# Performance work log

Measured on AMD Instinct MI355X. Metric: run time of the kernel, lower is better.

## Reference

```python
import jax, jax.numpy as jnp
import numpy as np

N_HEAD = 10

def setup_inputs() -> dict:
    key = jax.random.key(0)
    k1, k2, k3 = jax.random.split(key, 3)
    n_embd = 640
    x = jax.random.normal(k1, (4, 2048, n_embd), dtype=jnp.float32)
    w_qkv = jax.random.normal(k2, (3 * n_embd, n_embd), dtype=jnp.float32) * (1.0 / np.sqrt(n_embd))
    w_proj = jax.random.normal(k3, (n_embd, n_embd), dtype=jnp.float32) * (1.0 / np.sqrt(n_embd))
    return {"x": x, "w_qkv": w_qkv, "w_proj": w_proj}

def reference(x, w_qkv, w_proj):
    bsz, seqlen, n_embd = x.shape
    head_dim = n_embd // N_HEAD
    qkv = jnp.einsum('bsd,ed->bse', x, w_qkv)  # [B,S,3E]
    q, k, v = jnp.split(qkv, 3, axis=2)
    # [B,H,S,Dh]
    q = q.reshape(bsz, seqlen, N_HEAD, head_dim).transpose(0, 2, 1, 3)
    k = k.reshape(bsz, seqlen, N_HEAD, head_dim).transpose(0, 2, 1, 3)
    v = v.reshape(bsz, seqlen, N_HEAD, head_dim).transpose(0, 2, 1, 3)
    scale = 1.0 / np.sqrt(head_dim).astype(np.float32)
    scores = jnp.einsum('bhqd,bhkd->bhqk', q, k) * scale
    causal = jnp.tril(jnp.ones((seqlen, seqlen), dtype=bool))
    scores = jnp.where(causal, scores, jnp.finfo(scores.dtype).min)
    attn = jax.nn.softmax(scores, axis=-1)
    y = jnp.einsum('bhqk,bhkd->bhqd', attn, v)
    y = y.transpose(0, 2, 1, 3).reshape(bsz, seqlen, n_embd)
    return jnp.einsum('bsd,ed->bse', y, w_proj)
```

## Files before the change

### kernel.cpp

```cpp
#include <hip/hip_runtime.h>

#define BB 4
#define SS 2048
#define EE 640
#define NHH 10
#define DHH 64
#define MTOK 8192
#define E33 1920

#define LDST 72

typedef float f32x4 __attribute__((ext_vector_type(4)));
typedef __bf16 bf16x8 __attribute__((ext_vector_type(8)));
typedef unsigned short u16;
typedef u16 u16x4 __attribute__((ext_vector_type(4)));

__device__ inline u16 f2bf(float f) {
  unsigned u = __builtin_bit_cast(unsigned, f);
  u += 0x7fffu + ((u >> 16) & 1u);
  return (u16)(u >> 16);
}

__global__ void convert_kernel(const float* __restrict__ in, u16* __restrict__ out, int n4) {
  int i = blockIdx.x * blockDim.x + threadIdx.x;
  if (i < n4) {
    float4 v = ((const float4*)in)[i];
    u16x4 o = { f2bf(v.x), f2bf(v.y), f2bf(v.z), f2bf(v.w) };
    ((u16x4*)out)[i] = o;
  }
}

__global__ __launch_bounds__(256) void gemm_qkv(
    const u16* __restrict__ A, const u16* __restrict__ Bt,
    u16* __restrict__ qb, u16* __restrict__ kb, u16* __restrict__ vt) {
  __shared__ __align__(16) u16 As[128 * LDST];
  __shared__ __align__(16) u16 Bs[128 * LDST];
  const int t = threadIdx.x;
  const int m0 = blockIdx.y * 128;
  const int n0 = blockIdx.x * 128;
  const int w = t >> 6, lane = t & 63, n16 = lane & 15, quad = lane >> 4;
  const int wm = w >> 1, wn = w & 1;

  f32x4 acc[4][4];
  for (int i = 0; i < 4; i++)
    for (int j = 0; j < 4; j++) acc[i][j] = f32x4{0.f, 0.f, 0.f, 0.f};

  for (int kt = 0; kt < 10; ++kt) {
    __syncthreads();
    for (int i = 0; i < 4; ++i) {
      int c = i * 256 + t;
      int row = c >> 3, col0 = (c & 7) * 8;
      *(bf16x8*)&As[row * LDST + col0] = *(const bf16x8*)&A[(m0 + row) * 640 + kt * 64 + col0];
      *(bf16x8*)&Bs[row * LDST + col0] = *(const bf16x8*)&Bt[(n0 + row) * 640 + kt * 64 + col0];
    }
    __syncthreads();
    for (int ks = 0; ks < 2; ++ks) {
      bf16x8 a[4], b[4];
      for (int mi = 0; mi < 4; mi++)
        a[mi] = *(const bf16x8*)&As[(wm * 64 + mi * 16 + n16) * LDST + ks * 32 + quad * 8];
      for (int ni = 0; ni < 4; ni++)
        b[ni] = *(const bf16x8*)&Bs[(wn * 64 + ni * 16 + n16) * LDST + ks * 32 + quad * 8];
      for (int mi = 0; mi < 4; mi++)
        for (int ni = 0; ni < 4; ni++)
          acc[mi][ni] = __builtin_amdgcn_mfma_f32_16x16x32_bf16(a[mi], b[ni], acc[mi][ni], 0, 0, 0);
    }
  }

  const int which = n0 / 640;
  for (int ni = 0; ni < 4; ni++) {
    int col = n0 + wn * 64 + ni * 16 + n16;
    int eh = col - which * 640;
    int h = eh >> 6, d = eh & 63;
    for (int mi = 0; mi < 4; mi++) {
      int tb = m0 + wm * 64 + mi * 16 + quad * 4;
      f32x4 c = acc[mi][ni];
      if (which == 2) {
        int b_ = tb >> 11, s_ = tb & 2047;
        u16x4 pk = { f2bf(c[0]), f2bf(c[1]), f2bf(c[2]), f2bf(c[3]) };
        *(u16x4*)&vt[((b_ * NHH + h) * DHH + d) * SS + s_] = pk;
      } else {
        u16* dst = (which == 0) ? qb : kb;
        for (int r = 0; r < 4; r++) {
          int tok = tb + r;
          int b_ = tok >> 11, s_ = tok & 2047;
          dst[((b_ * NHH + h) * SS + s_) * DHH + d] = f2bf(c[r]);
        }
      }
    }
  }
}

__global__ __launch_bounds__(256) void attn_kernel(
    const u16* __restrict__ qb, const u16* __restrict__ kb, const u16* __restrict__ vt,
    u16* __restrict__ y) {
  __shared__ __align__(16) u16 Ks[2][64 * LDST];
  __shared__ __align__(16) u16 Vs[2][64 * LDST];
  const int t = threadIdx.x;
  const int w = t >> 6, lane = t & 63, n16 = lane & 15, quad = lane >> 4;
  const int bh = blockIdx.x;
  const int qt = 31 - blockIdx.y;
  const int qb0 = qt * 64;
  const int b_ = bh / NHH, h = bh % NHH;

  bf16x8 aq[2];
  {
    const u16* qp = &qb[(bh * SS + qb0 + w * 16 + n16) * DHH];
    aq[0] = *(const bf16x8*)&qp[quad * 8];
    aq[1] = *(const bf16x8*)&qp[32 + quad * 8];
  }
  const int q_rel = w * 16 + n16;

  const int c1 = 256 + t;
  const int row0 = t >> 3,  col0 = (t & 7) * 8;
  const int row1 = c1 >> 3, col1 = (c1 & 7) * 8;
  auto perm = [](int k) {
    int p = k >> 5, rem = k & 31, qd = rem >> 3, tt = rem & 7;
    return ((p << 1) | (tt >> 2)) * 16 + qd * 4 + (tt & 3);
  };
  const int prow0 = perm(row0), prow1 = perm(row1);

  float4 fk0, fk1, fv0, fv1;
  fk0 = *(const float4*)&kb[(bh * SS + row0) * DHH + col0];
  fk1 = *(const float4*)&kb[(bh * SS + row1) * DHH + col1];
  fv0 = *(const float4*)&vt[(bh * DHH + row0) * SS + col0];
  fv1 = *(const float4*)&vt[(bh * DHH + row1) * SS + col1];
  *(float4*)&Ks[0][prow0 * LDST + col0] = fk0;
  *(float4*)&Ks[0][prow1 * LDST + col1] = fk1;
  *(float4*)&Vs[0][row0 * LDST + col0] = fv0;
  *(float4*)&Vs[0][row1 * LDST + col1] = fv1;

  float m_i = -1e30f, l_i = 0.f;
  f32x4 o[4];
  for (int db = 0; db < 4; db++) o[db] = f32x4{0.f, 0.f, 0.f, 0.f};

  for (int kt = 0; kt <= qt; ++kt) {
    __syncthreads();
    const int cur = kt & 1, nxt = cur ^ 1;
    if (kt < qt) {
      int kk = (kt + 1) * 64;
      fk0 = *(const float4*)&kb[(bh * SS + kk + row0) * DHH + col0];
      fk1 = *(const float4*)&kb[(bh * SS + kk + row1) * DHH + col1];
      fv0 = *(const float4*)&vt[(bh * DHH + row0) * SS + kk + col0];
      fv1 = *(const float4*)&vt[(bh * DHH + row1) * SS + kk + col1];
    }

    f32x4 sc[4];
    for (int nb = 0; nb < 4; nb++) {
      f32x4 c = f32x4{0.f, 0.f, 0.f, 0.f};
      for (int ks = 0; ks < 2; ks++) {
        bf16x8 ak = *(const bf16x8*)&Ks[cur][(nb * 16 + n16) * LDST + ks * 32 + quad * 8];
        c = __builtin_amdgcn_mfma_f32_16x16x32_bf16(ak, aq[ks], c, 0, 0, 0);
      }
      sc[nb] = c;
    }
    const bool diag = (kt == qt);
    for (int nb = 0; nb < 4; nb++)
      for (int r = 0; r < 4; r++) {
        float v = sc[nb][r] * 0.125f;
        int key = ((nb >> 1) << 5) + quad * 8 + ((nb & 1) << 2) + r;
        sc[nb][r] = (diag && key > q_rel) ? -1e30f : v;
      }

    float rm = -1e30f;
    for (int nb = 0; nb < 4; nb++)
      for (int r = 0; r < 4; r++) rm = fmaxf(rm, sc[nb][r]);
    rm = fmaxf(rm, __shfl_xor(rm, 16));
    rm = fmaxf(rm, __shfl_xor(rm, 32));
    float mnew = fmaxf(m_i, rm);
    float alpha = __expf(m_i - mnew);
    float p[4][4];
    float rs = 0.f;
    for (int nb = 0; nb < 4; nb++)
      for (int r = 0; r < 4; r++) { float pv = __expf(sc[nb][r] - mnew); p[nb][r] = pv; rs += pv; }
    rs += __shfl_xor(rs, 16);
    rs += __shfl_xor(rs, 32);
    l_i = l_i * alpha + rs;
    m_i = mnew;
    for (int db = 0; db < 4; db++)
      for (int r = 0; r < 4; r++) o[db][r] *= alpha;

    for (int p2 = 0; p2 < 2; p2++) {
      union { bf16x8 v; u16 s[8]; } bp;
      for (int j = 0; j < 4; j++) {
        bp.s[j]     = f2bf(p[2 * p2][j]);
        bp.s[4 + j] = f2bf(p[2 * p2 + 1][j]);
      }
      for (int db = 0; db < 4; db++) {
        bf16x8 av = *(const bf16x8*)&Vs[cur][(db * 16 + n16) * LDST + p2 * 32 + quad * 8];
        o[db] = __builtin_amdgcn_mfma_f32_16x16x32_bf16(av, bp.v, o[db], 0, 0, 0);
      }
    }

    if (kt < qt) {
      *(float4*)&Ks[nxt][prow0 * LDST + col0] = fk0;
      *(float4*)&Ks[nxt][prow1 * LDST + col1] = fk1;
      *(float4*)&Vs[nxt][row0 * LDST + col0] = fv0;
      *(float4*)&Vs[nxt][row1 * LDST + col1] = fv1;
    }
  }

  const float inv = 1.0f / l_i;
  const int tok = b_ * SS + qb0 + w * 16 + n16;
  for (int db = 0; db < 4; db++) {
    u16x4 pk = { f2bf(o[db][0] * inv), f2bf(o[db][1] * inv),
                 f2bf(o[db][2] * inv), f2bf(o[db][3] * inv) };
    *(u16x4*)&y[tok * EE + h * DHH + db * 16 + quad * 4] = pk;
  }
}

__global__ __launch_bounds__(256) void gemm_proj(
    const u16* __restrict__ A, const u16* __restrict__ Bt, float* __restrict__ out) {
  __shared__ __align__(16) u16 As[128 * LDST];
  __shared__ __align__(16) u16 Bs[128 * LDST];
  const int t = threadIdx.x;
  const int m0 = blockIdx.y * 128;
  const int n0 = blockIdx.x * 128;
  const int w = t >> 6, lane = t & 63, n16 = lane & 15, quad = lane >> 4;
  const int wm = w >> 1, wn = w & 1;

  f32x4 acc[4][4];
  for (int i = 0; i < 4; i++)
    for (int j = 0; j < 4; j++) acc[i][j] = f32x4{0.f, 0.f, 0.f, 0.f};

  for (int kt = 0; kt < 10; ++kt) {
    __syncthreads();
    for (int i = 0; i < 4; ++i) {
      int c = i * 256 + t;
      int row = c >> 3, col0 = (c & 7) * 8;
      *(bf16x8*)&As[row * LDST + col0] = *(const bf16x8*)&A[(m0 + row) * 640 + kt * 64 + col0];
      *(bf16x8*)&Bs[row * LDST + col0] = *(const bf16x8*)&Bt[(n0 + row) * 640 + kt * 64 + col0];
    }
    __syncthreads();
    for (int ks = 0; ks < 2; ++ks) {
      bf16x8 a[4], b[4];
      for (int mi = 0; mi < 4; mi++)
        a[mi] = *(const bf16x8*)&As[(wm * 64 + mi * 16 + n16) * LDST + ks * 32 + quad * 8];
      for (int ni = 0; ni < 4; ni++)
        b[ni] = *(const bf16x8*)&Bs[(wn * 64 + ni * 16 + n16) * LDST + ks * 32 + quad * 8];
      for (int mi = 0; mi < 4; mi++)
        for (int ni = 0; ni < 4; ni++)
          acc[mi][ni] = __builtin_amdgcn_mfma_f32_16x16x32_bf16(a[mi], b[ni], acc[mi][ni], 0, 0, 0);
    }
  }

  for (int ni = 0; ni < 4; ni++) {
    int col = n0 + wn * 64 + ni * 16 + n16;
    for (int mi = 0; mi < 4; mi++) {
      int rowb = m0 + wm * 64 + mi * 16 + quad * 4;
      f32x4 c = acc[mi][ni];
      for (int r = 0; r < 4; r++) out[(rowb + r) * 640 + col] = c[r];
    }
  }
}

extern "C" void kernel_launch(void* const* d_in, const int* in_sizes, int n_in,
                              void* d_out, int out_size, void* d_ws, size_t ws_size,
                              hipStream_t stream) {
  const float* x     = (const float*)d_in[0];
  const float* wqkv  = (const float*)d_in[1];
  const float* wproj = (const float*)d_in[2];
  float* out = (float*)d_out;

  char* ws = (char*)d_ws;
  u16* xb     = (u16*)(ws + 0);
  u16* wqkvb  = (u16*)(ws + 10485760);
  u16* wprojb = (u16*)(ws + 12943360);
  u16* qbuf   = (u16*)(ws + 13762560);
  u16* kbuf   = (u16*)(ws + 24248320);
  u16* vtb    = (u16*)(ws + 34734080);
  u16* ybuf   = (u16*)(ws + 45219840);

  convert_kernel<<<5120, 256, 0, stream>>>(x, xb, 5242880 / 4);
  convert_kernel<<<1200, 256, 0, stream>>>(wqkv, wqkvb, 1228800 / 4);
  convert_kernel<<<400, 256, 0, stream>>>(wproj, wprojb, 409600 / 4);

  gemm_qkv<<<dim3(15, 64), 256, 0, stream>>>(xb, wqkvb, qbuf, kbuf, vtb);
  attn_kernel<<<dim3(40, 32), 256, 0, stream>>>(qbuf, kbuf, vtb, ybuf);
  gemm_proj<<<dim3(5, 64), 256, 0, stream>>>(ybuf, wprojb, out);
}
```

Before: 183.5 us.

## Use direct global-to-LDS loads, fold softmax scale into Q, merge conversions

Merges the three fp32-to-bf16 conversion launches into a single kernel. Both GEMMs now stage tiles with global_load_lds into an unpadded blocked LDS layout, and the projection GEMM uses 128x64 tiles, doubling its grid. The QKV GEMM writes Q transposed and pre-multiplied by scale*log2(e), so attention can use exp2 and skips the per-score multiply. Attention also masks only on the diagonal tile and packs P to bf16 with a perm instruction. The risks are a strided, uncoalesced transposed Q load in attention and possible LDS bank conflicts in the new layout.

Measured after the change: 192.0 us. 4.6% more time.

```diff
diff --git a/kernel.cpp b/kernel.cpp
--- a/kernel.cpp
+++ b/kernel.cpp
@@ -15,31 +15,60 @@
 typedef unsigned short u16;
 typedef u16 u16x4 __attribute__((ext_vector_type(4)));
 
+#define QSCALE 0.1803368801f
+
+#if __has_builtin(__builtin_amdgcn_exp2f)
+#define EXP2 __builtin_amdgcn_exp2f
+#else
+#define EXP2 exp2f
+#endif
+
 __device__ inline u16 f2bf(float f) {
   unsigned u = __builtin_bit_cast(unsigned, f);
   u += 0x7fffu + ((u >> 16) & 1u);
   return (u16)(u >> 16);
 }
 
-__global__ void convert_kernel(const float* __restrict__ in, u16* __restrict__ out, int n4) {
+__device__ inline unsigned pk2(float lo, float hi) {
+  unsigned a = __builtin_bit_cast(unsigned, lo) + 0x8000u;
+  unsigned b = __builtin_bit_cast(unsigned, hi) + 0x8000u;
+  return __builtin_amdgcn_perm(b, a, 0x07060302u);
+}
+
+__device__ inline void gll16(const u16* g, u16* l) {
+  __builtin_amdgcn_global_load_lds(
+      (const __attribute__((address_space(1))) unsigned*)g,
+      (__attribute__((address_space(3))) unsigned*)l, 16, 0, 0);
+}
+
+__global__ void convert_all(const float* __restrict__ x, const float* __restrict__ wqkv,
+                            const float* __restrict__ wproj, u16* __restrict__ xb,
+                            u16* __restrict__ wqkvb, u16* __restrict__ wprojb) {
   int i = blockIdx.x * blockDim.x + threadIdx.x;
-  if (i < n4) {
-    float4 v = ((const float4*)in)[i];
-    u16x4 o = { f2bf(v.x), f2bf(v.y), f2bf(v.z), f2bf(v.w) };
-    ((u16x4*)out)[i] = o;
-  }
+  const float* src; u16* dst; int off;
+  if (i < 1310720)      { src = x;     dst = xb;     off = i; }
+  else if (i < 1617920) { src = wqkv;  dst = wqkvb;  off = i - 1310720; }
+  else                  { src = wproj; dst = wprojb; off = i - 1617920; }
+  float4 v = ((const float4*)src)[off];
+  u16x4 o = { f2bf(v.x), f2bf(v.y), f2bf(v.z), f2bf(v.w) };
+  ((u16x4*)dst)[off] = o;
 }
 
 __global__ __launch_bounds__(256) void gemm_qkv(
     const u16* __restrict__ A, const u16* __restrict__ Bt,
-    u16* __restrict__ qb, u16* __restrict__ kb, u16* __restrict__ vt) {
-  __shared__ __align__(16) u16 As[128 * LDST];
-  __shared__ __align__(16) u16 Bs[128 * LDST];
-  const int t = threadIdx.x;
-  const int m0 = blockIdx.y * 128;
-  const int n0 = blockIdx.x * 128;
-  const int w = t >> 6, lane = t & 63, n16 = lane & 15, quad = lane >> 4;
+    u16* __restrict__ qT, u16* __restrict__ kb, u16* __restrict__ vt) {
+  __shared__ __align__(16) u16 As[128 * 64];
+  __shared__ __align__(16) u16 Bs[128 * 64];
+  const int t = threadIdx.x, w = t >> 6, lane = t & 63;
+  const int n16 = lane & 15, quad = lane >> 4;
   const int wm = w >> 1, wn = w & 1;
+  const int m0 = blockIdx.y * 128, n0 = blockIdx.x * 128;
+  const int mr = lane & 7, kc8 = (lane >> 3) * 8;
+
+  const u16* gA = A + (m0 + w * 32 + mr) * 640 + kc8;
+  const u16* gB = Bt + (n0 + w * 32 + mr) * 640 + kc8;
+  u16* lA = &As[w * 4 * 512];
+  u16* lB = &Bs[w * 4 * 512];
 
   f32x4 acc[4][4];
   for (int i = 0; i < 4; i++)
@@ -47,19 +76,21 @@
 
   for (int kt = 0; kt < 10; ++kt) {
     __syncthreads();
-    for (int i = 0; i < 4; ++i) {
-      int c = i * 256 + t;
-      int row = c >> 3, col0 = (c & 7) * 8;
-      *(bf16x8*)&As[row * LDST + col0] = *(const bf16x8*)&A[(m0 + row) * 640 + kt * 64 + col0];
-      *(bf16x8*)&Bs[row * LDST + col0] = *(const bf16x8*)&Bt[(n0 + row) * 640 + kt * 64 + col0];
+    for (int j = 0; j < 4; ++j) {
+      gll16(gA + j * 8 * 640 + kt * 64, lA + j * 512);
+      gll16(gB + j * 8 * 640 + kt * 64, lB + j * 512);
     }
     __syncthreads();
     for (int ks = 0; ks < 2; ++ks) {
       bf16x8 a[4], b[4];
-      for (int mi = 0; mi < 4; mi++)
-        a[mi] = *(const bf16x8*)&As[(wm * 64 + mi * 16 + n16) * LDST + ks * 32 + quad * 8];
-      for (int ni = 0; ni < 4; ni++)
-        b[ni] = *(const bf16x8*)&Bs[(wn * 64 + ni * 16 + n16) * LDST + ks * 32 + quad * 8];
+      for (int mi = 0; mi < 4; mi++) {
+        int m = wm * 64 + mi * 16 + n16;
+        a[mi] = *(const bf16x8*)&As[(m >> 3) * 512 + (ks * 4 + quad) * 64 + (m & 7) * 8];
+      }
+      for (int ni = 0; ni < 4; ni++) {
+        int n = wn * 64 + ni * 16 + n16;
+        b[ni] = *(const bf16x8*)&Bs[(n >> 3) * 512 + (ks * 4 + quad) * 64 + (n & 7) * 8];
+      }
       for (int mi = 0; mi < 4; mi++)
         for (int ni = 0; ni < 4; ni++)
           acc[mi][ni] = __builtin_amdgcn_mfma_f32_16x16x32_bf16(a[mi], b[ni], acc[mi][ni], 0, 0, 0);
@@ -73,25 +104,26 @@
     int h = eh >> 6, d = eh & 63;
     for (int mi = 0; mi < 4; mi++) {
       int tb = m0 + wm * 64 + mi * 16 + quad * 4;
+      int b_ = tb >> 11, s_ = tb & 2047;
+      int bh = b_ * NHH + h;
       f32x4 c = acc[mi][ni];
-      if (which == 2) {
-        int b_ = tb >> 11, s_ = tb & 2047;
+      if (which == 0) {
+        u16x4 pk = { f2bf(c[0] * QSCALE), f2bf(c[1] * QSCALE),
+                     f2bf(c[2] * QSCALE), f2bf(c[3] * QSCALE) };
+        *(u16x4*)&qT[(bh * DHH + d) * SS + s_] = pk;
+      } else if (which == 2) {
         u16x4 pk = { f2bf(c[0]), f2bf(c[1]), f2bf(c[2]), f2bf(c[3]) };
-        *(u16x4*)&vt[((b_ * NHH + h) * DHH + d) * SS + s_] = pk;
+        *(u16x4*)&vt[(bh * DHH + d) * SS + s_] = pk;
       } else {
-        u16* dst = (which == 0) ? qb : kb;
-        for (int r = 0; r < 4; r++) {
-          int tok = tb + r;
-          int b_ = tok >> 11, s_ = tok & 2047;
-          dst[((b_ * NHH + h) * SS + s_) * DHH + d] = f2bf(c[r]);
-        }
+        for (int r = 0; r < 4; r++)
+          kb[(bh * SS + s_ + r) * DHH + d] = f2bf(c[r]);
       }
     }
   }
 }
 
 __global__ __launch_bounds__(256) void attn_kernel(
-    const u16* __restrict__ qb, const u16* __restrict__ kb, const u16* __restrict__ vt,
+    const u16* __restrict__ qT, const u16* __restrict__ kb, const u16* __restrict__ vt,
     u16* __restrict__ y) {
   __shared__ __align__(16) u16 Ks[2][64 * LDST];
   __shared__ __align__(16) u16 Vs[2][64 * LDST];
@@ -101,14 +133,16 @@
   const int qt = 31 - blockIdx.y;
   const int qb0 = qt * 64;
   const int b_ = bh / NHH, h = bh % NHH;
+  const int q_rel = w * 16 + n16;
 
   bf16x8 aq[2];
   {
-    const u16* qp = &qb[(bh * SS + qb0 + w * 16 + n16) * DHH];
-    aq[0] = *(const bf16x8*)&qp[quad * 8];
-    aq[1] = *(const bf16x8*)&qp[32 + quad * 8];
-  }
-  const int q_rel = w * 16 + n16;
+    union { bf16x8 v; u16 s[8]; } u0, u1;
+    const u16* qp = qT + (bh * DHH) * SS + qb0 + q_rel;
+    for (int j = 0; j < 8; j++) u0.s[j] = qp[(quad * 8 + j) * SS];
+    for (int j = 0; j < 8; j++) u1.s[j] = qp[(32 + quad * 8 + j) * SS];
+    aq[0] = u0.v; aq[1] = u1.v;
+  }
 
   const int c1 = 256 + t;
   const int row0 = t >> 3,  col0 = (t & 7) * 8;
@@ -153,13 +187,13 @@
       }
       sc[nb] = c;
     }
-    const bool diag = (kt == qt);
-    for (int nb = 0; nb < 4; nb++)
-      for (int r = 0; r < 4; r++) {
-        float v = sc[nb][r] * 0.125f;
-        int key = ((nb >> 1) << 5) + quad * 8 + ((nb & 1) << 2) + r;
-        sc[nb][r] = (diag && key > q_rel) ? -1e30f : v;
-      }
+    if (kt == qt) {
+      for (int nb = 0; nb < 4; nb++)
+        for (int r = 0; r < 4; r++) {
+          int key = ((nb >> 1) << 5) + quad * 8 + ((nb & 1) << 2) + r;
+          if (key > q_rel) sc[nb][r] = -1e30f;
+        }
+    }
 
     float rm = -1e30f;
     for (int nb = 0; nb < 4; nb++)
@@ -167,11 +201,11 @@
     rm = fmaxf(rm, __shfl_xor(rm, 16));
     rm = fmaxf(rm, __shfl_xor(rm, 32));
     float mnew = fmaxf(m_i, rm);
-    float alpha = __expf(m_i - mnew);
+    float alpha = EXP2(m_i - mnew);
     float p[4][4];
     float rs = 0.f;
     for (int nb = 0; nb < 4; nb++)
-      for (int r = 0; r < 4; r++) { float pv = __expf(sc[nb][r] - mnew); p[nb][r] = pv; rs += pv; }
+      for (int r = 0; r < 4; r++) { float pv = EXP2(sc[nb][r] - mnew); p[nb][r] = pv; rs += pv; }
     rs += __shfl_xor(rs, 16);
     rs += __shfl_xor(rs, 32);
     l_i = l_i * alpha + rs;
@@ -180,11 +214,11 @@
       for (int r = 0; r < 4; r++) o[db][r] *= alpha;
 
     for (int p2 = 0; p2 < 2; p2++) {
-      union { bf16x8 v; u16 s[8]; } bp;
-      for (int j = 0; j < 4; j++) {
-        bp.s[j]     = f2bf(p[2 * p2][j]);
-        bp.s[4 + j] = f2bf(p[2 * p2 + 1][j]);
-      }
+      union { bf16x8 v; unsigned u[4]; } bp;
+      bp.u[0] = pk2(p[2 * p2][0],     p[2 * p2][1]);
+      bp.u[1] = pk2(p[2 * p2][2],     p[2 * p2][3]);
+      bp.u[2] = pk2(p[2 * p2 + 1][0], p[2 * p2 + 1][1]);
+      bp.u[3] = pk2(p[2 * p2 + 1][2], p[2 * p2 + 1][3]);
       for (int db = 0; db < 4; db++) {
         bf16x8 av = *(const bf16x8*)&Vs[cur][(db * 16 + n16) * LDST + p2 * 32 + quad * 8];
         o[db] = __builtin_amdgcn_mfma_f32_16x16x32_bf16(av, bp.v, o[db], 0, 0, 0);
@@ -210,43 +244,49 @@
 
 __global__ __launch_bounds__(256) void gemm_proj(
     const u16* __restrict__ A, const u16* __restrict__ Bt, float* __restrict__ out) {
-  __shared__ __align__(16) u16 As[128 * LDST];
-  __shared__ __align__(16) u16 Bs[128 * LDST];
-  const int t = threadIdx.x;
-  const int m0 = blockIdx.y * 128;
-  const int n0 = blockIdx.x * 128;
-  const int w = t >> 6, lane = t & 63, n16 = lane & 15, quad = lane >> 4;
-  const int wm = w >> 1, wn = w & 1;
-
-  f32x4 acc[4][4];
-  for (int i = 0; i < 4; i++)
+  __shared__ __align__(16) u16 As[128 * 64];
+  __shared__ __align__(16) u16 Bs[64 * 64];
+  const int t = threadIdx.x, w = t >> 6, lane = t & 63;
+  const int n16 = lane & 15, quad = lane >> 4;
+  const int m0 = blockIdx.y * 128, n0 = blockIdx.x * 64;
+  const int mr = lane & 7, kc8 = (lane >> 3) * 8;
+
+  const u16* gA = A + (m0 + w * 32 + mr) * 640 + kc8;
+  const u16* gB = Bt + (n0 + w * 16 + mr) * 640 + kc8;
+  u16* lA = &As[w * 4 * 512];
+  u16* lB = &Bs[w * 2 * 512];
+
+  f32x4 acc[2][4];
+  for (int i = 0; i < 2; i++)
     for (int j = 0; j < 4; j++) acc[i][j] = f32x4{0.f, 0.f, 0.f, 0.f};
 
   for (int kt = 0; kt < 10; ++kt) {
     __syncthreads();
-    for (int i = 0; i < 4; ++i) {
-      int c = i * 256 + t;
-      int row = c >> 3, col0 = (c & 7) * 8;
-      *(bf16x8*)&As[row * LDST + col0] = *(const bf16x8*)&A[(m0 + row) * 640 + kt * 64 + col0];
-      *(bf16x8*)&Bs[row * LDST + col0] = *(const bf16x8*)&Bt[(n0 + row) * 640 + kt * 64 + col0];
-    }
+    for (int j = 0; j < 4; ++j)
+      gll16(gA + j * 8 * 640 + kt * 64, lA + j * 512);
+    for (int j = 0; j < 2; ++j)
+      gll16(gB + j * 8 * 640 + kt * 64, lB + j * 512);
     __syncthreads();
     for (int ks = 0; ks < 2; ++ks) {
-      bf16x8 a[4], b[4];
-      for (int mi = 0; mi < 4; mi++)
-        a[mi] = *(const bf16x8*)&As[(wm * 64 + mi * 16 + n16) * LDST + ks * 32 + quad * 8];
-      for (int ni = 0; ni < 4; ni++)
-        b[ni] = *(const bf16x8*)&Bs[(wn * 64 + ni * 16 + n16) * LDST + ks * 32 + quad * 8];
-      for (int mi = 0; mi < 4; mi++)
+      bf16x8 a[2], b[4];
+      for (int mi = 0; mi < 2; mi++) {
+        int m = w * 32 + mi * 16 + n16;
+        a[mi] = *(const bf16x8*)&As[(m >> 3) * 512 + (ks * 4 + quad) * 64 + (m & 7) * 8];
+      }
+      for (int ni = 0; ni < 4; ni++) {
+        int n = ni * 16 + n16;
+        b[ni] = *(const bf16x8*)&Bs[(n >> 3) * 512 + (ks * 4 + quad) * 64 + (n & 7) * 8];
+      }
+      for (int mi = 0; mi < 2; mi++)
         for (int ni = 0; ni < 4; ni++)
           acc[mi][ni] = __builtin_amdgcn_mfma_f32_16x16x32_bf16(a[mi], b[ni], acc[mi][ni], 0, 0, 0);
     }
   }
 
   for (int ni = 0; ni < 4; ni++) {
-    int col = n0 + wn * 64 + ni * 16 + n16;
-    for (int mi = 0; mi < 4; mi++) {
-      int rowb = m0 + wm * 64 + mi * 16 + quad * 4;
+    int col = n0 + ni * 16 + n16;
+    for (int mi = 0; mi < 2; mi++) {
+      int rowb = m0 + w * 32 + mi * 16 + quad * 4;
       f32x4 c = acc[mi][ni];
       for (int r = 0; r < 4; r++) out[(rowb + r) * 640 + col] = c[r];
     }
@@ -265,16 +305,13 @@
   u16* xb     = (u16*)(ws + 0);
   u16* wqkvb  = (u16*)(ws + 10485760);
   u16* wprojb = (u16*)(ws + 12943360);
-  u16* qbuf   = (u16*)(ws + 13762560);
+  u16* qTb    = (u16*)(ws + 13762560);
   u16* kbuf   = (u16*)(ws + 24248320);
   u16* vtb    = (u16*)(ws + 34734080);
   u16* ybuf   = (u16*)(ws + 45219840);
 
-  convert_kernel<<<5120, 256, 0, stream>>>(x, xb, 5242880 / 4);
-  convert_kernel<<<1200, 256, 0, stream>>>(wqkv, wqkvb, 1228800 / 4);
-  convert_kernel<<<400, 256, 0, stream>>>(wproj, wprojb, 409600 / 4);
-
-  gemm_qkv<<<dim3(15, 64), 256, 0, stream>>>(xb, wqkvb, qbuf, kbuf, vtb);
-  attn_kernel<<<dim3(40, 32), 256, 0, stream>>>(qbuf, kbuf, vtb, ybuf);
-  gemm_proj<<<dim3(5, 64), 256, 0, stream>>>(ybuf, wprojb, out);
-}
+  convert_all<<<6720, 256, 0, stream>>>(x, wqkv, wproj, xb, wqkvb, wprojb);
+  gemm_qkv<<<dim3(15, 64), 256, 0, stream>>>(xb, wqkvb, qTb, kbuf, vtb);
+  attn_kernel<<<dim3(40, 32), 256, 0, stream>>>(qTb, kbuf, vtb, ybuf);
+  gemm_proj<<<dim3(10, 64), 256, 0, stream>>>(ybuf, wprojb, out);
+}
```
